# Optimization experiments

Hardware: AMD Instinct MI355X
Metric: run time of the kernel (lower is better)

The kernel has to match this reference:

```python
import jax, jax.numpy as jnp
import numpy as np

H = 64  # hidden dim
D_IN = 15  # per-step feature dim


def _gru_layer(x, Wih, Whh, bih, bhh):
    """torch-style GRU, batch_first. x: [M, T, D] -> [M, T, H]."""
    xp = x @ Wih.T + bih  # [M, T, 3H], precomputed input projections

    def step(h, xt):
        gh = h @ Whh.T + bhh
        xr, xz, xn = jnp.split(xt, 3, axis=-1)
        hr, hz, hn = jnp.split(gh, 3, axis=-1)
        r = jax.nn.sigmoid(xr + hr)
        z = jax.nn.sigmoid(xz + hz)
        n = jnp.tanh(xn + r * hn)
        h_new = (1.0 - z) * n + z * h
        return h_new, h_new

    h0 = jnp.zeros((x.shape[0], Whh.shape[1]), x.dtype)
    _, hs = jax.lax.scan(step, h0, jnp.swapaxes(xp, 0, 1))  # [T, M, H]
    return jnp.swapaxes(hs, 0, 1)


def setup_inputs() -> dict:
    key = jax.random.key(0)
    ks = jax.random.split(key, 16)
    N, B, T = 500, 32, 32
    s = 0.05
    return {
        "raw": jax.random.normal(ks[0], (N, B, T, D_IN), dtype=jnp.float32),
        # GRU layer 1 (input 15 -> 64)
        "gru1_Wih": jax.random.normal(ks[1], (3 * H, D_IN), dtype=jnp.float32) * s,
        "gru1_Whh": jax.random.normal(ks[2], (3 * H, H), dtype=jnp.float32) * s,
        "gru1_bih": jax.random.normal(ks[3], (3 * H,), dtype=jnp.float32) * s,
        "gru1_bhh": jax.random.normal(ks[4], (3 * H,), dtype=jnp.float32) * s,
        # GRU layer 2 (64 -> 64)
        "gru2_Wih": jax.random.normal(ks[5], (3 * H, H), dtype=jnp.float32) * s,
        "gru2_Whh": jax.random.normal(ks[6], (3 * H, H), dtype=jnp.float32) * s,
        "gru2_bih": jax.random.normal(ks[7], (3 * H,), dtype=jnp.float32) * s,
        "gru2_bhh": jax.random.normal(ks[8], (3 * H,), dtype=jnp.float32) * s,
        # temporal attention fc (64 -> 1)
        "attn_W": jax.random.normal(ks[9], (1, H), dtype=jnp.float32) * s,
        "attn_b": jax.random.normal(ks[10], (1,), dtype=jnp.float32) * s,
        # GAT attention-block linear W (64 -> 64) and u (128,)
        "gat_W_w": jax.random.normal(ks[11], (H, H), dtype=jnp.float32) * s,
        "gat_W_b": jax.random.normal(ks[12], (H,), dtype=jnp.float32) * s,
        "gat_u": jax.random.normal(ks[13], (2 * H,), dtype=jnp.float32) * s,
        # GAT value projection W1 (64 -> 64)
        "gat_W1_w": jax.random.normal(ks[14], (H, H), dtype=jnp.float32) * s,
        "gat_W1_b": jax.random.normal(ks[15], (H,), dtype=jnp.float32) * s,
    }


def reference(raw, gru1_Wih, gru1_Whh, gru1_bih, gru1_bhh,
              gru2_Wih, gru2_Whh, gru2_bih, gru2_bhh,
              attn_W, attn_b, gat_W_w, gat_W_b, gat_u, gat_W1_w, gat_W1_b):
    N, B, T, D = raw.shape
    x = raw.reshape(N * B, T, D)

    # SequenceEncoder: two stacked GRUs + temporal attention (dropout = eval identity)
    h = _gru_layer(x, gru1_Wih, gru1_Whh, gru1_bih, gru1_bhh)
    h = _gru_layer(h, gru2_Wih, gru2_Whh, gru2_bih, gru2_bhh)  # [NB, T, H]
    scores = jnp.tanh(h @ attn_W.T + attn_b)                    # [NB, T, 1]
    w = jax.nn.softmax(scores, axis=1)                          # softmax over time
    Ai = jnp.sum(h * w, axis=1).reshape(N, B, H)                # [N, B, H]

    # GAT over all-to-all node graph
    sq = Ai @ gat_W_w.T + gat_W_b          # attention-block projection [N, B, H]
    s_q = sq @ gat_u[:H]                   # query-side score [N, B]
    s_k = sq @ gat_u[H:]                   # neighbor-side score [N, B]
    score = s_q[:, None, :] + s_k[None, :, :]                   # [Nq, Nk, B]
    beta = jnp.exp(jax.nn.leaky_relu(score, negative_slope=0.01))
    beta = beta / jnp.sum(beta, axis=1, keepdims=True)          # normalize over neighbors
    proj = Ai @ gat_W1_w.T + gat_W1_b                           # value projection [N, B, H]
    g = jax.nn.relu(jnp.einsum('qkb,kbd->qbd', beta, proj))     # [N, B, H]
    return g
```

## Files before the change

kernel.cpp:

```cpp
#include <hip/hip_runtime.h>

#define TT 32
#define DIN 15
#define LOG2E 1.44269504088896340736f

typedef _Float16 f16x8 __attribute__((ext_vector_type(8)));
typedef _Float16 f16x4 __attribute__((ext_vector_type(4)));
typedef float f32x4 __attribute__((ext_vector_type(4)));

__device__ __forceinline__ float rcp_(float x){ return __builtin_amdgcn_rcpf(x); }
__device__ __forceinline__ float exp2_(float x){ return __builtin_amdgcn_exp2f(x); }
__device__ __forceinline__ float tanh_(float x){ return fmaf(-2.f, rcp_(__expf(2.f*x)+1.f), 1.f); }

#define MFMA(a,b,c) __builtin_amdgcn_mfma_f32_16x16x32_f16(a,b,c,0,0,0)

__device__ __forceinline__ f16x8 f16x8_zero(){
  f16x8 v;
  #pragma unroll
  for (int j=0;j<8;++j) v[j]=(_Float16)0.f;
  return v;
}

__global__ void wprep(const float* __restrict__ w1ih, const float* __restrict__ w1hh,
                      const float* __restrict__ w2ih, const float* __restrict__ w2hh,
                      const float* __restrict__ b1ih, const float* __restrict__ b1hh,
                      const float* __restrict__ W1,
                      const float* __restrict__ Ww, const float* __restrict__ Wb,
                      const float* __restrict__ u,
                      _Float16* __restrict__ wf, float* __restrict__ vqk){
  int id = blockIdx.x*256 + threadIdx.x;
  if (id < 47104){
    int e = id & 7, c = id >> 3;
    float v, scale;
    if (c < 4608){
      int mat = c / 1536; int r = c - mat*1536;
      int lane = r & 63, kf = (r>>6)&1, q = r>>7;
      const float* W = (mat==0)? w1hh : (mat==1)? w2ih : w2hh;
      int ht = q/3, g3 = q - ht*3;
      int row = g3*64 + ht*16 + (lane & 15);
      int k = kf*32 + (lane>>4)*8 + e;
      v = W[row*64 + k];
      scale = (g3==2) ? 2.f*LOG2E : -LOG2E;
    } else if (c < 5376){
      int r = c - 4608; int lane = r & 63, q = r>>6;
      int ht = q/3, g3 = q - ht*3;
      int row = g3*64 + ht*16 + (lane & 15);
      int k = (lane>>4)*8 + e;
      if (k < DIN)       v = w1ih[row*DIN + k];
      else if (k == DIN) v = (g3 < 2) ? (b1ih[row] + b1hh[row]) : b1ih[row];
      else               v = 0.f;
      scale = (g3==2) ? 2.f*LOG2E : -LOG2E;
    } else {
      int r = c - 5376; int lane = r & 63, q = r>>6;
      int ht = q>>1, kf = q&1;
      int row = ht*16 + (lane & 15);
      int k = kf*32 + (lane>>4)*8 + e;
      v = W1[row*64 + k]; scale = 1.f;
    }
    wf[c*8 + e] = (_Float16)(v*scale);
  } else if (id < 47104 + 130){
    int t = id - 47104;
    if (t < 128){
      int which = t>>6, j = t&63;
      float s = 0.f;
      for (int i=0;i<64;++i) s = fmaf(u[which*64+i], Ww[i*64+j], s);
      vqk[t] = s;
    } else {
      int which = t-128;
      float s = 0.f;
      for (int i=0;i<64;++i) s = fmaf(u[which*64+i], Wb[i], s);
      vqk[128+which] = s;
    }
  }
}

__global__ __launch_bounds__(256, 2) void gru_mfma(
    const float* __restrict__ raw,
    const _Float16* __restrict__ wf,
    const float* __restrict__ vqk,
    const float* __restrict__ bhh1,
    const float* __restrict__ bih2, const float* __restrict__ bhh2,
    const float* __restrict__ attnW, const float* __restrict__ attnb,
    const float* __restrict__ W1b,
    _Float16* __restrict__ projh, float* __restrict__ sqT, float* __restrict__ skT)
{
  __shared__ _Float16 xfh[TT*64*8];
  __shared__ _Float16 h1s[32*64];
  __shared__ _Float16 h2s[32*64];
  __shared__ float bias2[256];
  __shared__ float attp[2][4][16];
  __shared__ float attq[4][32], attk[4][32];

  const int tid  = threadIdx.x;
  const int lane = tid & 63;
  const int ht   = tid >> 6;
  const int g    = lane >> 4;
  const int sl   = lane & 15;
  const int s7   = sl & 7;
  const int n    = blockIdx.x;
  const int seq0 = n*32;
  const int row0 = ht*16 + g*4;

  { int* z2 = (int*)h2s; for (int i=tid; i<1024; i+=256) z2[i]=0; }
  if (tid < 64){
    bias2[tid]       = -(bih2[tid]      + bhh2[tid])   *LOG2E;
    bias2[64+tid]    = -(bih2[64+tid]   + bhh2[64+tid])*LOG2E;
    bias2[128+tid]   =  bih2[128+tid]*(2.f*LOG2E);
    bias2[192+tid]   =  bhh2[128+tid]*(2.f*LOG2E);
  }
  for (int idx=tid; idx<TT*32; idx+=256){
    int s = idx & 31, t = idx >> 5;
    const float* rp = &raw[(size_t)(seq0+s)*(TT*DIN) + t*DIN];
    f16x8 lo, hi;
    #pragma unroll
    for (int j=0;j<8;++j){
      lo[j] = (_Float16)rp[j];
      hi[j] = (j<7) ? (_Float16)rp[8+j] : (_Float16)1.0f;
    }
    *(f16x8*)(xfh + ((size_t)t*64 +      s)*8) = lo;
    *(f16x8*)(xfh + ((size_t)t*64 + 32 + s)*8) = hi;
  }

  const f16x8* wf8 = (const f16x8*)wf;
  f16x8 wr1_0 = wf8[((ht*3+0)*2+0)*64 + lane], wr1_1 = wf8[((ht*3+0)*2+1)*64 + lane];
  f16x8 wz1_0 = wf8[((ht*3+1)*2+0)*64 + lane], wz1_1 = wf8[((ht*3+1)*2+1)*64 + lane];
  f16x8 wn1_0 = wf8[((ht*3+2)*2+0)*64 + lane], wn1_1 = wf8[((ht*3+2)*2+1)*64 + lane];
  f16x8 ar2_0 = wf8[1536+((ht*3+0)*2+0)*64 + lane], ar2_1 = wf8[1536+((ht*3+0)*2+1)*64 + lane];
  f16x8 az2_0 = wf8[1536+((ht*3+1)*2+0)*64 + lane], az2_1 = wf8[1536+((ht*3+1)*2+1)*64 + lane];
  f16x8 an2_0 = wf8[1536+((ht*3+2)*2+0)*64 + lane], an2_1 = wf8[1536+((ht*3+2)*2+1)*64 + lane];
  f16x8 br2_0 = wf8[3072+((ht*3+0)*2+0)*64 + lane], br2_1 = wf8[3072+((ht*3+0)*2+1)*64 + lane];
  f16x8 bz2_0 = wf8[3072+((ht*3+1)*2+0)*64 + lane], bz2_1 = wf8[3072+((ht*3+1)*2+1)*64 + lane];
  f16x8 bn2_0 = wf8[3072+((ht*3+2)*2+0)*64 + lane], bn2_1 = wf8[3072+((ht*3+2)*2+1)*64 + lane];
  f16x8 xr1 = wf8[4608 + (ht*3+0)*64 + lane];
  f16x8 xz1 = wf8[4608 + (ht*3+1)*64 + lane];
  f16x8 xn1 = wf8[4608 + (ht*3+2)*64 + lane];

  f32x4 Bhn1, awv;
  #pragma unroll
  for (int r=0;r<4;++r){ Bhn1[r] = bhh1[128+row0+r]*(2.f*LOG2E); awv[r] = attnW[row0+r]; }
  const float ab = attnb[0];

  __syncthreads();

  const f16x8 fz = f16x8_zero();
  f16x8 h1f0_0=fz, h1f0_1=fz, h1f1_0=fz, h1f1_1=fz;
  f32x4 h1c0={0,0,0,0}, h1c1={0,0,0,0}, h2c0={0,0,0,0}, h2c1={0,0,0,0};
  f32x4 num0={0,0,0,0}, num1={0,0,0,0};
  float den0=0.f, den1=0.f;

  #pragma unroll 1
  for (int t=0; t<TT; ++t){
    f16x8 xf0 = fz, xf1 = fz;
    if (g < 2){
      xf0 = *(const f16x8*)(xfh + ((size_t)t*64 + g*32 +      sl)*8);
      xf1 = *(const f16x8*)(xfh + ((size_t)t*64 + g*32 + 16 + sl)*8);
    }
    f16x8 h2f0_0 = *(const f16x8*)(h2s + sl*64      + ((g    ^s7))*8);
    f16x8 h2f0_1 = *(const f16x8*)(h2s + sl*64      + (((4+g)^s7))*8);
    f16x8 h2f1_0 = *(const f16x8*)(h2s + (16+sl)*64 + ((g    ^s7))*8);
    f16x8 h2f1_1 = *(const f16x8*)(h2s + (16+sl)*64 + (((4+g)^s7))*8);
    if (t > 0){
      float s40 = attp[0][0][sl]+attp[0][1][sl]+attp[0][2][sl]+attp[0][3][sl];
      float s41 = attp[1][0][sl]+attp[1][1][sl]+attp[1][2][sl]+attp[1][3][sl];
      float e0 = __expf(tanh_(s40 + ab));
      float e1 = __expf(tanh_(s41 + ab));
      den0 += e0; den1 += e1;
      #pragma unroll
      for (int r=0;r<4;++r){
        num0[r] = fmaf(e0, h2c0[r], num0[r]);
        num1[r] = fmaf(e1, h2c1[r], num1[r]);
      }
    }
    f32x4 Cr0={0,0,0,0}, Cz0={0,0,0,0}, Cxn0={0,0,0,0}, Chn0=Bhn1;
    f32x4 Cr1={0,0,0,0}, Cz1={0,0,0,0}, Cxn1={0,0,0,0}, Chn1=Bhn1;
    Cr0 = MFMA(wr1_0,h1f0_0,Cr0); Cr0 = MFMA(wr1_1,h1f0_1,Cr0); Cr0 = MFMA(xr1,xf0,Cr0);
    Cr1 = MFMA(wr1_0,h1f1_0,Cr1); Cr1 = MFMA(wr1_1,h1f1_1,Cr1); Cr1 = MFMA(xr1,xf1,Cr1);
    Cz0 = MFMA(wz1_0,h1f0_0,Cz0); Cz0 = MFMA(wz1_1,h1f0_1,Cz0); Cz0 = MFMA(xz1,xf0,Cz0);
    Cz1 = MFMA(wz1_0,h1f1_0,Cz1); Cz1 = MFMA(wz1_1,h1f1_1,Cz1); Cz1 = MFMA(xz1,xf1,Cz1);
    Chn0 = MFMA(wn1_0,h1f0_0,Chn0); Chn0 = MFMA(wn1_1,h1f0_1,Chn0);
    Chn1 = MFMA(wn1_0,h1f1_0,Chn1); Chn1 = MFMA(wn1_1,h1f1_1,Chn1);
    Cxn0 = MFMA(xn1,xf0,Cxn0);
    Cxn1 = MFMA(xn1,xf1,Cxn1);
    f16x4 hw0, hw1;
    #pragma unroll
    for (int r=0;r<4;++r){
      float rg0 = rcp_(1.f + exp2_(Cr0[r]));
      float zg0 = rcp_(1.f + exp2_(Cz0[r]));
      float ng0 = fmaf(-2.f, rcp_(exp2_(Cxn0[r] + rg0*Chn0[r]) + 1.f), 1.f);
      float h0  = ng0 + zg0*(h1c0[r] - ng0);
      h1c0[r] = h0; hw0[r] = (_Float16)h0;
      float rg1 = rcp_(1.f + exp2_(Cr1[r]));
      float zg1 = rcp_(1.f + exp2_(Cz1[r]));
      float ng1 = fmaf(-2.f, rcp_(exp2_(Cxn1[r] + rg1*Chn1[r]) + 1.f), 1.f);
      float h1v = ng1 + zg1*(h1c1[r] - ng1);
      h1c1[r] = h1v; hw1[r] = (_Float16)h1v;
    }
    { const int cw = (((ht*2+(g>>1)) ^ s7))*8 + (g&1)*4;
      *(f16x4*)(h1s + sl*64      + cw) = hw0;
      *(f16x4*)(h1s + (16+sl)*64 + cw) = hw1; }
    __syncthreads();
    h1f0_0 = *(const f16x8*)(h1s + sl*64      + ((g    ^s7))*8);
    h1f0_1 = *(const f16x8*)(h1s + sl*64      + (((4+g)^s7))*8);
    h1f1_0 = *(const f16x8*)(h1s + (16+sl)*64 + ((g    ^s7))*8);
    h1f1_1 = *(const f16x8*)(h1s + (16+sl)*64 + (((4+g)^s7))*8);
    f32x4 Dr0  = *(const f32x4*)(bias2 + row0);
    f32x4 Dz0  = *(const f32x4*)(bias2 + 64 + row0);
    f32x4 Dxn0 = *(const f32x4*)(bias2 + 128 + row0);
    f32x4 Dhn0 = *(const f32x4*)(bias2 + 192 + row0);
    f32x4 Dr1 = Dr0, Dz1 = Dz0, Dxn1 = Dxn0, Dhn1 = Dhn0;
    Dr0  = MFMA(ar2_0,h1f0_0,Dr0);  Dr0  = MFMA(ar2_1,h1f0_1,Dr0);
    Dr0  = MFMA(br2_0,h2f0_0,Dr0);  Dr0  = MFMA(br2_1,h2f0_1,Dr0);
    Dr1  = MFMA(ar2_0,h1f1_0,Dr1);  Dr1  = MFMA(ar2_1,h1f1_1,Dr1);
    Dr1  = MFMA(br2_0,h2f1_0,Dr1);  Dr1  = MFMA(br2_1,h2f1_1,Dr1);
    Dz0  = MFMA(az2_0,h1f0_0,Dz0);  Dz0  = MFMA(az2_1,h1f0_1,Dz0);
    Dz0  = MFMA(bz2_0,h2f0_0,Dz0);  Dz0  = MFMA(bz2_1,h2f0_1,Dz0);
    Dz1  = MFMA(az2_0,h1f1_0,Dz1);  Dz1  = MFMA(az2_1,h1f1_1,Dz1);
    Dz1  = MFMA(bz2_0,h2f1_0,Dz1);  Dz1  = MFMA(bz2_1,h2f1_1,Dz1);
    Dxn0 = MFMA(an2_0,h1f0_0,Dxn0); Dxn0 = MFMA(an2_1,h1f0_1,Dxn0);
    Dxn1 = MFMA(an2_0,h1f1_0,Dxn1); Dxn1 = MFMA(an2_1,h1f1_1,Dxn1);
    Dhn0 = MFMA(bn2_0,h2f0_0,Dhn0); Dhn0 = MFMA(bn2_1,h2f0_1,Dhn0);
    Dhn1 = MFMA(bn2_0,h2f1_0,Dhn1); Dhn1 = MFMA(bn2_1,h2f1_1,Dhn1);
    float p0 = 0.f, p1 = 0.f;
    #pragma unroll
    for (int r=0;r<4;++r){
      float rg0 = rcp_(1.f + exp2_(Dr0[r]));
      float zg0 = rcp_(1.f + exp2_(Dz0[r]));
      float ng0 = fmaf(-2.f, rcp_(exp2_(Dxn0[r] + rg0*Dhn0[r]) + 1.f), 1.f);
      float h0  = ng0 + zg0*(h2c0[r] - ng0);
      h2c0[r] = h0; hw0[r] = (_Float16)h0;
      p0 = fmaf(h0, awv[r], p0);
      float rg1 = rcp_(1.f + exp2_(Dr1[r]));
      float zg1 = rcp_(1.f + exp2_(Dz1[r]));
      float ng1 = fmaf(-2.f, rcp_(exp2_(Dxn1[r] + rg1*Dhn1[r]) + 1.f), 1.f);
      float h1v = ng1 + zg1*(h2c1[r] - ng1);
      h2c1[r] = h1v; hw1[r] = (_Float16)h1v;
      p1 = fmaf(h1v, awv[r], p1);
    }
    { const int cw = (((ht*2+(g>>1)) ^ s7))*8 + (g&1)*4;
      *(f16x4*)(h2s + sl*64      + cw) = hw0;
      *(f16x4*)(h2s + (16+sl)*64 + cw) = hw1; }
    p0 += __shfl_xor(p0, 16, 64); p0 += __shfl_xor(p0, 32, 64);
    p1 += __shfl_xor(p1, 16, 64); p1 += __shfl_xor(p1, 32, 64);
    if (lane < 16){ attp[0][ht][sl] = p0; attp[1][ht][sl] = p1; }
    __syncthreads();
  }
  {
    float s40 = attp[0][0][sl]+attp[0][1][sl]+attp[0][2][sl]+attp[0][3][sl];
    float s41 = attp[1][0][sl]+attp[1][1][sl]+attp[1][2][sl]+attp[1][3][sl];
    float e0 = __expf(tanh_(s40 + ab));
    float e1 = __expf(tanh_(s41 + ab));
    den0 += e0; den1 += e1;
    #pragma unroll
    for (int r=0;r<4;++r){
      num0[r] = fmaf(e0, h2c0[r], num0[r]);
      num1[r] = fmaf(e1, h2c1[r], num1[r]);
    }
  }
  float rd0 = rcp_(den0), rd1 = rcp_(den1);
  f32x4 av0, av1;
  #pragma unroll
  for (int r=0;r<4;++r){ av0[r] = num0[r]*rd0; av1[r] = num1[r]*rd1; }
  {
    f32x4 vq4 = *(const f32x4*)&vqk[row0];
    f32x4 vk4 = *(const f32x4*)&vqk[64+row0];
    float pq0=0.f, pk0=0.f, pq1=0.f, pk1=0.f;
    #pragma unroll
    for (int r=0;r<4;++r){
      pq0 = fmaf(av0[r], vq4[r], pq0); pk0 = fmaf(av0[r], vk4[r], pk0);
      pq1 = fmaf(av1[r], vq4[r], pq1); pk1 = fmaf(av1[r], vk4[r], pk1);
    }
    pq0 += __shfl_xor(pq0,16,64); pq0 += __shfl_xor(pq0,32,64);
    pk0 += __shfl_xor(pk0,16,64); pk0 += __shfl_xor(pk0,32,64);
    pq1 += __shfl_xor(pq1,16,64); pq1 += __shfl_xor(pq1,32,64);
    pk1 += __shfl_xor(pk1,16,64); pk1 += __shfl_xor(pk1,32,64);
    if (lane < 16){
      attq[ht][sl] = pq0;    attk[ht][sl] = pk0;
      attq[ht][16+sl] = pq1; attk[ht][16+sl] = pk1;
    }
  }
  { f16x4 af0, af1;
    #pragma unroll
    for (int r=0;r<4;++r){ af0[r] = (_Float16)av0[r]; af1[r] = (_Float16)av1[r]; }
    const int cw = (((ht*2+(g>>1)) ^ s7))*8 + (g&1)*4;
    *(f16x4*)(h1s + sl*64      + cw) = af0;
    *(f16x4*)(h1s + (16+sl)*64 + cw) = af1; }
  __syncthreads();
  if (tid < 32){
    float q4 = attq[0][tid]+attq[1][tid]+attq[2][tid]+attq[3][tid];
    float k4 = attk[0][tid]+attk[1][tid]+attk[2][tid]+attk[3][tid];
    sqT[tid*512 + n] = (q4 + vqk[128])*LOG2E;
    skT[tid*512 + n] = (k4 + vqk[129])*LOG2E;
  }
  {
    f16x8 a0 = wf8[5376 + (ht*2+0)*64 + lane];
    f16x8 a1 = wf8[5376 + (ht*2+1)*64 + lane];
    f16x8 b00 = *(const f16x8*)(h1s + sl*64      + ((g    ^s7))*8);
    f16x8 b01 = *(const f16x8*)(h1s + sl*64      + (((4+g)^s7))*8);
    f16x8 b10 = *(const f16x8*)(h1s + (16+sl)*64 + ((g    ^s7))*8);
    f16x8 b11 = *(const f16x8*)(h1s + (16+sl)*64 + (((4+g)^s7))*8);
    f32x4 P0 = *(const f32x4*)&W1b[row0];
    f32x4 P1 = P0;
    P0 = MFMA(a0,b00,P0); P0 = MFMA(a1,b01,P0);
    P1 = MFMA(a0,b10,P1); P1 = MFMA(a1,b11,P1);
    f16x4 pf0, pf1;
    #pragma unroll
    for (int r=0;r<4;++r){ pf0[r] = (_Float16)P0[r]; pf1[r] = (_Float16)P1[r]; }
    *(f16x4*)(projh + (size_t)(seq0+sl)*64    + row0) = pf0;
    *(f16x4*)(projh + (size_t)(seq0+16+sl)*64 + row0) = pf1;
  }
}

__global__ __launch_bounds__(256) void gat_agg(
    const _Float16* __restrict__ projh,
    const float* __restrict__ sqT, const float* __restrict__ skT,
    float* __restrict__ out)
{
  __shared__ _Float16 pT[64*64];
  __shared__ float sks[512];
  const int tid  = threadIdx.x;
  const int lane = tid & 63;
  const int wv   = tid >> 6;
  const int b    = blockIdx.x & 31;
  const int qt   = blockIdx.x >> 5;
  const int sl   = lane & 15, g = lane >> 4;
  const int myq  = qt*64 + wv*16 + sl;
  const float sq_l = (myq < 500) ? sqT[b*512 + myq] : -1e30f;
  for (int j = tid; j < 512; j += 256) sks[j] = (j < 500) ? skT[b*512 + j] : -1e30f;

  f32x4 acc[4] = {{0,0,0,0},{0,0,0,0},{0,0,0,0},{0,0,0,0}};
  float den_l = 0.f;
  const int kr = tid & 63, dgrp = tid >> 6;

  f16x8 pv0 = f16x8_zero(), pv1 = f16x8_zero();
  if (kr < 500){
    const f16x8* pp = (const f16x8*)(projh + ((size_t)kr*32 + b)*64 + dgrp*16);
    pv0 = pp[0]; pv1 = pp[1];
  }

  #pragma unroll 1
  for (int kc=0; kc<8; ++kc){
    __syncthreads();
    { char* base = (char*)pT;
      const int klo = (kr & 7) << 1, khi = kr >> 3;
      #pragma unroll
      for (int j=0;j<16;++j){
        int d = dgrp*16 + j;
        _Float16 v = (j<8) ? pv0[j] : pv1[j-8];
        *(_Float16*)(base + d*128 + (((khi ^ (d&7))) << 4) + klo) = v;
      } }
    __syncthreads();
    if (kc < 7){
      int node = (kc+1)*64 + kr;
      if (node < 500){
        const f16x8* pp = (const f16x8*)(projh + ((size_t)node*32 + b)*64 + dgrp*16);
        pv0 = pp[0]; pv1 = pp[1];
      } else { pv0 = f16x8_zero(); pv1 = f16x8_zero(); }
    }
    #pragma unroll
    for (int kc32=0; kc32<2; ++kc32){
      const int kb = kc*64 + kc32*32 + g*8;
      float4 skv0 = *(const float4*)&sks[kb];
      float4 skv1 = *(const float4*)&sks[kb+4];
      float s[8] = {sq_l+skv0.x, sq_l+skv0.y, sq_l+skv0.z, sq_l+skv0.w,
                    sq_l+skv1.x, sq_l+skv1.y, sq_l+skv1.z, sq_l+skv1.w};
      f16x8 bf;
      #pragma unroll
      for (int e=0;e<8;++e){
        float sc = fmaxf(s[e], 0.01f*s[e]);
        float ev = exp2_(sc);
        den_l += ev;
        bf[e] = (_Float16)ev;
      }
      const char* base = (const char*)pT;
      #pragma unroll
      for (int dt=0; dt<4; ++dt){
        f16x8 a = *(const f16x8*)(base + (dt*16 + sl)*128 + (((kc32*4 + g) ^ (sl&7)) << 4));
        acc[dt] = MFMA(a, bf, acc[dt]);
      }
    }
  }
  den_l += __shfl_xor(den_l, 16, 64);
  den_l += __shfl_xor(den_l, 32, 64);
  const float rd = rcp_(den_l);
  if (myq < 500){
    #pragma unroll
    for (int dt=0; dt<4; ++dt){
      f32x4 o;
      #pragma unroll
      for (int r=0;r<4;++r) o[r] = fmaxf(acc[dt][r]*rd, 0.f);
      *(f32x4*)&out[((size_t)myq*32 + b)*64 + dt*16 + g*4] = o;
    }
  }
}

extern "C" void kernel_launch(void* const* d_in, const int* in_sizes, int n_in,
                              void* d_out, int out_size, void* d_ws, size_t ws_size,
                              hipStream_t stream) {
  const float* raw   = (const float*)d_in[0];
  const float* w1ih  = (const float*)d_in[1];
  const float* w1hh  = (const float*)d_in[2];
  const float* b1ih  = (const float*)d_in[3];
  const float* b1hh  = (const float*)d_in[4];
  const float* w2ih  = (const float*)d_in[5];
  const float* w2hh  = (const float*)d_in[6];
  const float* b2ih  = (const float*)d_in[7];
  const float* b2hh  = (const float*)d_in[8];
  const float* attW  = (const float*)d_in[9];
  const float* attb  = (const float*)d_in[10];
  const float* gWw   = (const float*)d_in[11];
  const float* gWb   = (const float*)d_in[12];
  const float* gu    = (const float*)d_in[13];
  const float* gW1   = (const float*)d_in[14];
  const float* gW1b  = (const float*)d_in[15];
  float* outp = (float*)d_out;

  char* wsb = (char*)d_ws;
  _Float16* projh = (_Float16*)wsb;
  float*    sqT   = (float*)(wsb + 2048000);
  float*    skT   = (float*)(wsb + 2048000 + 65536);
  _Float16* wfh   = (_Float16*)(wsb + 2048000 + 131072);
  float*    vqk   = (float*)(wsb + 2048000 + 131072 + 94208);

  wprep<<<185, 256, 0, stream>>>(w1ih, w1hh, w2ih, w2hh, b1ih, b1hh,
                                 gW1, gWw, gWb, gu, wfh, vqk);
  gru_mfma<<<500, 256, 0, stream>>>(raw, wfh, vqk, b1hh, b2ih, b2hh,
                                    attW, attb, gW1b, projh, sqT, skT);
  gat_agg<<<256, 256, 0, stream>>>(projh, sqT, skT, outp);
}
```

Before: 89.43 us.

## Skew GRU layers by one step with double-buffered LDS, one barrier per step

```diff
diff --git a/kernel.cpp b/kernel.cpp
--- a/kernel.cpp
+++ b/kernel.cpp
@@ -85,10 +85,10 @@
     _Float16* __restrict__ projh, float* __restrict__ sqT, float* __restrict__ skT)
 {
   __shared__ _Float16 xfh[TT*64*8];
-  __shared__ _Float16 h1s[32*64];
-  __shared__ _Float16 h2s[32*64];
+  __shared__ _Float16 h1s[2][32*64];
+  __shared__ _Float16 h2s[2][32*64];
   __shared__ float bias2[256];
-  __shared__ float attp[2][4][16];
+  __shared__ float attp[2][2][4][16];
   __shared__ float attq[4][32], attk[4][32];
 
   const int tid  = threadIdx.x;
@@ -101,7 +101,7 @@
   const int seq0 = n*32;
   const int row0 = ht*16 + g*4;
 
-  { int* z2 = (int*)h2s; for (int i=tid; i<1024; i+=256) z2[i]=0; }
+  { int* z2 = (int*)h2s[0]; for (int i=tid; i<1024; i+=256) z2[i]=0; }
   if (tid < 64){
     bias2[tid]       = -(bih2[tid]      + bhh2[tid])   *LOG2E;
     bias2[64+tid]    = -(bih2[64+tid]   + bhh2[64+tid])*LOG2E;
@@ -143,25 +143,64 @@
   __syncthreads();
 
   const f16x8 fz = f16x8_zero();
-  f16x8 h1f0_0=fz, h1f0_1=fz, h1f1_0=fz, h1f1_1=fz;
   f32x4 h1c0={0,0,0,0}, h1c1={0,0,0,0}, h2c0={0,0,0,0}, h2c1={0,0,0,0};
   f32x4 num0={0,0,0,0}, num1={0,0,0,0};
   float den0=0.f, den1=0.f;
-
-  #pragma unroll 1
-  for (int t=0; t<TT; ++t){
+  const int cwr = (((ht*2+(g>>1)) ^ s7))*8 + (g&1)*4;
+
+  {
     f16x8 xf0 = fz, xf1 = fz;
     if (g < 2){
-      xf0 = *(const f16x8*)(xfh + ((size_t)t*64 + g*32 +      sl)*8);
-      xf1 = *(const f16x8*)(xfh + ((size_t)t*64 + g*32 + 16 + sl)*8);
-    }
-    f16x8 h2f0_0 = *(const f16x8*)(h2s + sl*64      + ((g    ^s7))*8);
-    f16x8 h2f0_1 = *(const f16x8*)(h2s + sl*64      + (((4+g)^s7))*8);
-    f16x8 h2f1_0 = *(const f16x8*)(h2s + (16+sl)*64 + ((g    ^s7))*8);
-    f16x8 h2f1_1 = *(const f16x8*)(h2s + (16+sl)*64 + (((4+g)^s7))*8);
-    if (t > 0){
-      float s40 = attp[0][0][sl]+attp[0][1][sl]+attp[0][2][sl]+attp[0][3][sl];
-      float s41 = attp[1][0][sl]+attp[1][1][sl]+attp[1][2][sl]+attp[1][3][sl];
+      xf0 = *(const f16x8*)(xfh + ((size_t)0*64 + g*32 +      sl)*8);
+      xf1 = *(const f16x8*)(xfh + ((size_t)0*64 + g*32 + 16 + sl)*8);
+    }
+    f32x4 Cr0={0,0,0,0}, Cz0={0,0,0,0}, Cxn0={0,0,0,0}, Chn0=Bhn1;
+    f32x4 Cr1={0,0,0,0}, Cz1={0,0,0,0}, Cxn1={0,0,0,0}, Chn1=Bhn1;
+    Cr0 = MFMA(xr1,xf0,Cr0); Cz0 = MFMA(xz1,xf0,Cz0); Cxn0 = MFMA(xn1,xf0,Cxn0);
+    Cr1 = MFMA(xr1,xf1,Cr1); Cz1 = MFMA(xz1,xf1,Cz1); Cxn1 = MFMA(xn1,xf1,Cxn1);
+    f16x4 hw0, hw1;
+    #pragma unroll
+    for (int r=0;r<4;++r){
+      float rg0 = rcp_(1.f + exp2_(Cr0[r]));
+      float zg0 = rcp_(1.f + exp2_(Cz0[r]));
+      float ng0 = fmaf(-2.f, rcp_(exp2_(Cxn0[r] + rg0*Chn0[r]) + 1.f), 1.f);
+      float h0  = ng0 - zg0*ng0;
+      h1c0[r] = h0; hw0[r] = (_Float16)h0;
+      float rg1 = rcp_(1.f + exp2_(Cr1[r]));
+      float zg1 = rcp_(1.f + exp2_(Cz1[r]));
+      float ng1 = fmaf(-2.f, rcp_(exp2_(Cxn1[r] + rg1*Chn1[r]) + 1.f), 1.f);
+      float h1v = ng1 - zg1*ng1;
+      h1c1[r] = h1v; hw1[r] = (_Float16)h1v;
+    }
+    *(f16x4*)(h1s[0] + sl*64      + cwr) = hw0;
+    *(f16x4*)(h1s[0] + (16+sl)*64 + cwr) = hw1;
+  }
+  __syncthreads();
+
+  #pragma unroll 1
+  for (int i=0; i<TT; ++i){
+    const _Float16* h1rd = h1s[i&1];
+    const _Float16* h2rd = h2s[i&1];
+    _Float16* h1wr = h1s[(i+1)&1];
+    _Float16* h2wr = h2s[(i+1)&1];
+    f16x8 h1f0_0 = *(const f16x8*)(h1rd + sl*64      + ((g    ^s7))*8);
+    f16x8 h1f0_1 = *(const f16x8*)(h1rd + sl*64      + (((4+g)^s7))*8);
+    f16x8 h1f1_0 = *(const f16x8*)(h1rd + (16+sl)*64 + ((g    ^s7))*8);
+    f16x8 h1f1_1 = *(const f16x8*)(h1rd + (16+sl)*64 + (((4+g)^s7))*8);
+    f16x8 h2f0_0 = *(const f16x8*)(h2rd + sl*64      + ((g    ^s7))*8);
+    f16x8 h2f0_1 = *(const f16x8*)(h2rd + sl*64      + (((4+g)^s7))*8);
+    f16x8 h2f1_0 = *(const f16x8*)(h2rd + (16+sl)*64 + ((g    ^s7))*8);
+    f16x8 h2f1_1 = *(const f16x8*)(h2rd + (16+sl)*64 + (((4+g)^s7))*8);
+    const int tn = (i < TT-1) ? i+1 : TT-1;
+    f16x8 xf0 = fz, xf1 = fz;
+    if (g < 2){
+      xf0 = *(const f16x8*)(xfh + ((size_t)tn*64 + g*32 +      sl)*8);
+      xf1 = *(const f16x8*)(xfh + ((size_t)tn*64 + g*32 + 16 + sl)*8);
+    }
+    if (i > 0){
+      const float (*ap)[4][16] = attp[(i+1)&1];
+      float s40 = ap[0][0][sl]+ap[0][1][sl]+ap[0][2][sl]+ap[0][3][sl];
+      float s41 = ap[1][0][sl]+ap[1][1][sl]+ap[1][2][sl]+ap[1][3][sl];
       float e0 = __expf(tanh_(s40 + ab));
       float e1 = __expf(tanh_(s41 + ab));
       den0 += e0; den1 += e1;
@@ -171,38 +210,6 @@
         num1[r] = fmaf(e1, h2c1[r], num1[r]);
       }
     }
-    f32x4 Cr0={0,0,0,0}, Cz0={0,0,0,0}, Cxn0={0,0,0,0}, Chn0=Bhn1;
-    f32x4 Cr1={0,0,0,0}, Cz1={0,0,0,0}, Cxn1={0,0,0,0}, Chn1=Bhn1;
-    Cr0 = MFMA(wr1_0,h1f0_0,Cr0); Cr0 = MFMA(wr1_1,h1f0_1,Cr0); Cr0 = MFMA(xr1,xf0,Cr0);
-    Cr1 = MFMA(wr1_0,h1f1_0,Cr1); Cr1 = MFMA(wr1_1,h1f1_1,Cr1); Cr1 = MFMA(xr1,xf1,Cr1);
-    Cz0 = MFMA(wz1_0,h1f0_0,Cz0); Cz0 = MFMA(wz1_1,h1f0_1,Cz0); Cz0 = MFMA(xz1,xf0,Cz0);
-    Cz1 = MFMA(wz1_0,h1f1_0,Cz1); Cz1 = MFMA(wz1_1,h1f1_1,Cz1); Cz1 = MFMA(xz1,xf1,Cz1);
-    Chn0 = MFMA(wn1_0,h1f0_0,Chn0); Chn0 = MFMA(wn1_1,h1f0_1,Chn0);
-    Chn1 = MFMA(wn1_0,h1f1_0,Chn1); Chn1 = MFMA(wn1_1,h1f1_1,Chn1);
-    Cxn0 = MFMA(xn1,xf0,Cxn0);
-    Cxn1 = MFMA(xn1,xf1,Cxn1);
-    f16x4 hw0, hw1;
-    #pragma unroll
-    for (int r=0;r<4;++r){
-      float rg0 = rcp_(1.f + exp2_(Cr0[r]));
-      float zg0 = rcp_(1.f + exp2_(Cz0[r]));
-      float ng0 = fmaf(-2.f, rcp_(exp2_(Cxn0[r] + rg0*Chn0[r]) + 1.f), 1.f);
-      float h0  = ng0 + zg0*(h1c0[r] - ng0);
-      h1c0[r] = h0; hw0[r] = (_Float16)h0;
-      float rg1 = rcp_(1.f + exp2_(Cr1[r]));
-      float zg1 = rcp_(1.f + exp2_(Cz1[r]));
-      float ng1 = fmaf(-2.f, rcp_(exp2_(Cxn1[r] + rg1*Chn1[r]) + 1.f), 1.f);
-      float h1v = ng1 + zg1*(h1c1[r] - ng1);
-      h1c1[r] = h1v; hw1[r] = (_Float16)h1v;
-    }
-    { const int cw = (((ht*2+(g>>1)) ^ s7))*8 + (g&1)*4;
-      *(f16x4*)(h1s + sl*64      + cw) = hw0;
-      *(f16x4*)(h1s + (16+sl)*64 + cw) = hw1; }
-    __syncthreads();
-    h1f0_0 = *(const f16x8*)(h1s + sl*64      + ((g    ^s7))*8);
-    h1f0_1 = *(const f16x8*)(h1s + sl*64      + (((4+g)^s7))*8);
-    h1f1_0 = *(const f16x8*)(h1s + (16+sl)*64 + ((g    ^s7))*8);
-    h1f1_1 = *(const f16x8*)(h1s + (16+sl)*64 + (((4+g)^s7))*8);
     f32x4 Dr0  = *(const f32x4*)(bias2 + row0);
     f32x4 Dz0  = *(const f32x4*)(bias2 + 64 + row0);
     f32x4 Dxn0 = *(const f32x4*)(bias2 + 128 + row0);
@@ -220,6 +227,17 @@
     Dxn1 = MFMA(an2_0,h1f1_0,Dxn1); Dxn1 = MFMA(an2_1,h1f1_1,Dxn1);
     Dhn0 = MFMA(bn2_0,h2f0_0,Dhn0); Dhn0 = MFMA(bn2_1,h2f0_1,Dhn0);
     Dhn1 = MFMA(bn2_0,h2f1_0,Dhn1); Dhn1 = MFMA(bn2_1,h2f1_1,Dhn1);
+    f32x4 Cr0={0,0,0,0}, Cz0={0,0,0,0}, Cxn0={0,0,0,0}, Chn0=Bhn1;
+    f32x4 Cr1={0,0,0,0}, Cz1={0,0,0,0}, Cxn1={0,0,0,0}, Chn1=Bhn1;
+    Cr0 = MFMA(wr1_0,h1f0_0,Cr0); Cr0 = MFMA(wr1_1,h1f0_1,Cr0); Cr0 = MFMA(xr1,xf0,Cr0);
+    Cr1 = MFMA(wr1_0,h1f1_0,Cr1); Cr1 = MFMA(wr1_1,h1f1_1,Cr1); Cr1 = MFMA(xr1,xf1,Cr1);
+    Cz0 = MFMA(wz1_0,h1f0_0,Cz0); Cz0 = MFMA(wz1_1,h1f0_1,Cz0); Cz0 = MFMA(xz1,xf0,Cz0);
+    Cz1 = MFMA(wz1_0,h1f1_0,Cz1); Cz1 = MFMA(wz1_1,h1f1_1,Cz1); Cz1 = MFMA(xz1,xf1,Cz1);
+    Chn0 = MFMA(wn1_0,h1f0_0,Chn0); Chn0 = MFMA(wn1_1,h1f0_1,Chn0);
+    Chn1 = MFMA(wn1_0,h1f1_0,Chn1); Chn1 = MFMA(wn1_1,h1f1_1,Chn1);
+    Cxn0 = MFMA(xn1,xf0,Cxn0);
+    Cxn1 = MFMA(xn1,xf1,Cxn1);
+    f16x4 hw0, hw1;
     float p0 = 0.f, p1 = 0.f;
     #pragma unroll
     for (int r=0;r<4;++r){
@@ -236,17 +254,34 @@
       h2c1[r] = h1v; hw1[r] = (_Float16)h1v;
       p1 = fmaf(h1v, awv[r], p1);
     }
-    { const int cw = (((ht*2+(g>>1)) ^ s7))*8 + (g&1)*4;
-      *(f16x4*)(h2s + sl*64      + cw) = hw0;
-      *(f16x4*)(h2s + (16+sl)*64 + cw) = hw1; }
+    *(f16x4*)(h2wr + sl*64      + cwr) = hw0;
+    *(f16x4*)(h2wr + (16+sl)*64 + cwr) = hw1;
     p0 += __shfl_xor(p0, 16, 64); p0 += __shfl_xor(p0, 32, 64);
     p1 += __shfl_xor(p1, 16, 64); p1 += __shfl_xor(p1, 32, 64);
-    if (lane < 16){ attp[0][ht][sl] = p0; attp[1][ht][sl] = p1; }
+    if (lane < 16){ attp[i&1][0][ht][sl] = p0; attp[i&1][1][ht][sl] = p1; }
+    if (i < TT-1){
+      #pragma unroll
+      for (int r=0;r<4;++r){
+        float rg0 = rcp_(1.f + exp2_(Cr0[r]));
+        float zg0 = rcp_(1.f + exp2_(Cz0[r]));
+        float ng0 = fmaf(-2.f, rcp_(exp2_(Cxn0[r] + rg0*Chn0[r]) + 1.f), 1.f);
+        float h0  = ng0 + zg0*(h1c0[r] - ng0);
+        h1c0[r] = h0; hw0[r] = (_Float16)h0;
+        float rg1 = rcp_(1.f + exp2_(Cr1[r]));
+        float zg1 = rcp_(1.f + exp2_(Cz1[r]));
+        float ng1 = fmaf(-2.f, rcp_(exp2_(Cxn1[r] + rg1*Chn1[r]) + 1.f), 1.f);
+        float h1v = ng1 + zg1*(h1c1[r] - ng1);
+        h1c1[r] = h1v; hw1[r] = (_Float16)h1v;
+      }
+      *(f16x4*)(h1wr + sl*64      + cwr) = hw0;
+      *(f16x4*)(h1wr + (16+sl)*64 + cwr) = hw1;
+    }
     __syncthreads();
   }
   {
-    float s40 = attp[0][0][sl]+attp[0][1][sl]+attp[0][2][sl]+attp[0][3][sl];
-    float s41 = attp[1][0][sl]+attp[1][1][sl]+attp[1][2][sl]+attp[1][3][sl];
+    const float (*ap)[4][16] = attp[1];
+    float s40 = ap[0][0][sl]+ap[0][1][sl]+ap[0][2][sl]+ap[0][3][sl];
+    float s41 = ap[1][0][sl]+ap[1][1][sl]+ap[1][2][sl]+ap[1][3][sl];
     float e0 = __expf(tanh_(s40 + ab));
     float e1 = __expf(tanh_(s41 + ab));
     den0 += e0; den1 += e1;
@@ -281,9 +316,8 @@
   { f16x4 af0, af1;
     #pragma unroll
     for (int r=0;r<4;++r){ af0[r] = (_Float16)av0[r]; af1[r] = (_Float16)av1[r]; }
-    const int cw = (((ht*2+(g>>1)) ^ s7))*8 + (g&1)*4;
-    *(f16x4*)(h1s + sl*64      + cw) = af0;
-    *(f16x4*)(h1s + (16+sl)*64 + cw) = af1; }
+    *(f16x4*)(h1s[0] + sl*64      + cwr) = af0;
+    *(f16x4*)(h1s[0] + (16+sl)*64 + cwr) = af1; }
   __syncthreads();
   if (tid < 32){
     float q4 = attq[0][tid]+attq[1][tid]+attq[2][tid]+attq[3][tid];
@@ -294,10 +328,10 @@
   {
     f16x8 a0 = wf8[5376 + (ht*2+0)*64 + lane];
     f16x8 a1 = wf8[5376 + (ht*2+1)*64 + lane];
-    f16x8 b00 = *(const f16x8*)(h1s + sl*64      + ((g    ^s7))*8);
-    f16x8 b01 = *(const f16x8*)(h1s + sl*64      + (((4+g)^s7))*8);
-    f16x8 b10 = *(const f16x8*)(h1s + (16+sl)*64 + ((g    ^s7))*8);
-    f16x8 b11 = *(const f16x8*)(h1s + (16+sl)*64 + (((4+g)^s7))*8);
+    f16x8 b00 = *(const f16x8*)(h1s[0] + sl*64      + ((g    ^s7))*8);
+    f16x8 b01 = *(const f16x8*)(h1s[0] + sl*64      + (((4+g)^s7))*8);
+    f16x8 b10 = *(const f16x8*)(h1s[0] + (16+sl)*64 + ((g    ^s7))*8);
+    f16x8 b11 = *(const f16x8*)(h1s[0] + (16+sl)*64 + (((4+g)^s7))*8);
     f32x4 P0 = *(const f32x4*)&W1b[row0];
     f32x4 P1 = P0;
     P0 = MFMA(a0,b00,P0); P0 = MFMA(a1,b01,P0);
```

Result: slower. 92.24 us (+3.1%).
